# Performance work log

Hardware: AMD Instinct MI355X
Metric: run time of the kernel (lower is better)

## Reference

```python
import jax, jax.numpy as jnp
import numpy as np

N = 100000   # nodes
E = 1600000  # directed edges
D = 128      # feature dim (input = hidden = embedding)
LN_EPS = 1e-5


def setup_inputs() -> dict:
    key = jax.random.key(0)
    ks = jax.random.split(key, 8)
    scale = 1.0 / np.sqrt(D)
    x = jax.random.normal(ks[0], (N, D), dtype=jnp.float32)
    edge_index = jax.random.randint(ks[1], (2, E), 0, N, dtype=jnp.int64)
    W0 = jax.random.normal(ks[2], (D, D), dtype=jnp.float32) * scale
    W1 = jax.random.normal(ks[3], (D, D), dtype=jnp.float32) * scale
    W2 = jax.random.normal(ks[4], (D, D), dtype=jnp.float32) * scale
    b0 = jnp.zeros((D,), jnp.float32)
    b1 = jnp.zeros((D,), jnp.float32)
    b2 = jnp.zeros((D,), jnp.float32)
    ln_g = jnp.ones((D,), jnp.float32)
    ln_b = jnp.zeros((D,), jnp.float32)
    fn_g = jnp.ones((D,), jnp.float32)
    fn_b = jnp.zeros((D,), jnp.float32)
    return {"x": x, "edge_index": edge_index, "W0": W0, "b0": b0,
            "W1": W1, "b1": b1, "W2": W2, "b2": b2,
            "ln_g": ln_g, "ln_b": ln_b, "fn_g": fn_g, "fn_b": fn_b}


def _gcn_conv(x, W, b, src, dst, n):
    # PyG GCNConv: x' = D^{-1/2} (A + I) D^{-1/2} (x W) + b
    h = x @ W                                   # [N, D]
    # add self-loops
    loops = jnp.arange(n, dtype=src.dtype)
    s = jnp.concatenate([src, loops])           # source nodes
    d = jnp.concatenate([dst, loops])           # target nodes
    deg = jax.ops.segment_sum(jnp.ones_like(d, dtype=h.dtype), d, num_segments=n)
    dinv = jnp.where(deg > 0, jax.lax.rsqrt(deg), 0.0)
    norm = dinv[s] * dinv[d]                    # [E+N]
    msg = h[s] * norm[:, None]                  # gather + scale
    out = jax.ops.segment_sum(msg, d, num_segments=n)  # scatter-add at targets
    return out + b


def _layer_norm(x, g, b):
    mu = jnp.mean(x, axis=-1, keepdims=True)
    var = jnp.mean(jnp.square(x - mu), axis=-1, keepdims=True)
    return (x - mu) * jax.lax.rsqrt(var + LN_EPS) * g + b


def reference(x, edge_index, W0, b0, W1, b1, W2, b2, ln_g, ln_b, fn_g, fn_b):
    src, dst = edge_index[0], edge_index[1]
    n = x.shape[0]
    h = jax.nn.relu(_gcn_conv(x, W0, b0, src, dst, n))
    # single middle block (num_gnn_layers=3 -> loop runs for i=1 only)
    identity = h
    h = _layer_norm(h, ln_g, ln_b)
    h = jax.nn.relu(_gcn_conv(h, W1, b1, src, dst, n)) + identity
    h = _gcn_conv(h, W2, b2, src, dst, n)
    return _layer_norm(h, fn_g, fn_b)
```

## Files before the change

### kernel.cpp

```cpp
#include <hip/hip_runtime.h>
#include <hip/hip_bf16.h>

#define DIM 128
#define SB 256
#define NA 256
#define EAMAX 6272
#define BCAP 4096

typedef __attribute__((ext_vector_type(8))) short bf16x8;
typedef __attribute__((ext_vector_type(4))) float f32x4;

__device__ inline float bf2f(unsigned short u) {
    unsigned v = (unsigned)u << 16;
    union { unsigned u; float f; } c; c.u = v; return c.f;
}
__device__ inline unsigned short f2bf(float f) {
    union { __hip_bfloat16 h; unsigned short u; } c;
    c.h = __float2bfloat16(f);
    return c.u;
}
__device__ inline unsigned pk2(float a, float b) {
    return (unsigned)f2bf(a) | ((unsigned)f2bf(b) << 16);
}


__global__ __launch_bounds__(256) void k_hist(const int* __restrict__ dst,
                                              int* __restrict__ histG,
                                              int E, int EA, int nbuk) {
    __shared__ int h[1024];
    int t = threadIdx.x, blk = blockIdx.x;
    for (int i = t; i < 1024; i += 256) h[i] = 0;
    __syncthreads();
    int lo = blk * EA, hi = min(E, lo + EA);
    for (int i = lo + t; i < hi; i += 256) atomicAdd(&h[dst[i] >> 7], 1);
    __syncthreads();
    for (int bk = t; bk < nbuk; bk += 256) histG[bk * NA + blk] = h[bk];
}

__global__ __launch_bounds__(SB) void k_scan1(const int* __restrict__ cnt,
                                              int* __restrict__ bsum, int n) {
    int t = threadIdx.x;
    int i = blockIdx.x * SB + t;
    int v = (i < n) ? cnt[i] : 0;
#pragma unroll
    for (int m = 1; m < 64; m <<= 1) v += __shfl_xor(v, m);
    __shared__ int w[SB / 64];
    if ((t & 63) == 0) w[t >> 6] = v;
    __syncthreads();
    if (t == 0) {
        int s = 0;
#pragma unroll
        for (int k = 0; k < SB / 64; ++k) s += w[k];
        bsum[blockIdx.x] = s;
    }
}

__global__ __launch_bounds__(1024) void k_scan2(int* __restrict__ bsum, int B) {
    __shared__ int s[1024];
    int t = threadIdx.x;
    int v = (t < B) ? bsum[t] : 0;
    s[t] = v;
    __syncthreads();
    for (int off = 1; off < 1024; off <<= 1) {
        int u = (t >= off) ? s[t - off] : 0;
        __syncthreads();
        s[t] += u;
        __syncthreads();
    }
    if (t < B) bsum[t] = s[t] - v;
}

__global__ __launch_bounds__(SB) void k_scan3g(const int* __restrict__ cnt,
                                               const int* __restrict__ bsum,
                                               int* __restrict__ outx, int n) {
    __shared__ int s[SB];
    int t = threadIdx.x;
    int i = blockIdx.x * SB + t;
    int c = (i < n) ? cnt[i] : 0;
    s[t] = c;
    __syncthreads();
    for (int off = 1; off < SB; off <<= 1) {
        int u = (t >= off) ? s[t - off] : 0;
        __syncthreads();
        s[t] += u;
        __syncthreads();
    }
    int excl = bsum[blockIdx.x] + s[t] - c;
    if (i < n) {
        outx[i] = excl;
        if (i == n - 1) outx[n] = excl + c;
    }
}

__global__ __launch_bounds__(256) void k_place(const int* __restrict__ src,
                                               const int* __restrict__ dst,
                                               const int* __restrict__ scannedG,
                                               unsigned* __restrict__ ebuf,
                                               int E, int EA, int nbuk) {
    __shared__ int h[1024];
    __shared__ int dl[1024];
    __shared__ int ws4[4];
    __shared__ unsigned srt[EAMAX];
    __shared__ unsigned short bkt[EAMAX];
    int t = threadIdx.x, blk = blockIdx.x;
    int lo = blk * EA, hi = min(E, lo + EA);

    for (int i = t; i < 1024; i += 256) h[i] = 0;
    __syncthreads();
    for (int i = lo + t; i < hi; i += 256) atomicAdd(&h[dst[i] >> 7], 1);
    __syncthreads();

    {
        int b4 = t * 4;
        int v0 = h[b4], v1 = h[b4 + 1], v2 = h[b4 + 2], v3 = h[b4 + 3];
        int i1 = v0 + v1, i2 = i1 + v2, i3 = i2 + v3;
        int lane = t & 63, wv = t >> 6;
        int sc = i3;
#pragma unroll
        for (int o = 1; o < 64; o <<= 1) {
            int u = __shfl_up(sc, o);
            if (lane >= o) sc += u;
        }
        if (lane == 63) ws4[wv] = sc;
        __syncthreads();
        int woff = 0;
#pragma unroll
        for (int k = 0; k < 4; ++k) woff += (k < wv) ? ws4[k] : 0;
        int tex = woff + sc - i3;
        h[b4] = tex; h[b4 + 1] = tex + v0; h[b4 + 2] = tex + i1; h[b4 + 3] = tex + i2;
    }
    __syncthreads();

    for (int bk = t; bk < nbuk; bk += 256)
        dl[bk] = scannedG[bk * NA + blk] - h[bk];
    __syncthreads();

    for (int i = lo + t; i < hi; i += 256) {
        int d = dst[i];
        int bk = d >> 7;
        unsigned p = ((unsigned)(d & 127) << 17) | (unsigned)src[i];
        int r = atomicAdd(&h[bk], 1);
        srt[r] = p;
        bkt[r] = (unsigned short)bk;
    }
    __syncthreads();

    int m = hi - lo;
    for (int i = t; i < m; i += 256)
        ebuf[dl[bkt[i]] + i] = srt[i];
}

__global__ __launch_bounds__(256) void k_finish(const unsigned* __restrict__ ebuf,
                                                const int* __restrict__ scannedG,
                                                int* __restrict__ offs,
                                                float* __restrict__ dinv,
                                                int* __restrict__ csrc,
                                                int n, int nbuk) {
    __shared__ unsigned eds[BCAP];
    __shared__ unsigned srt[BCAP];
    __shared__ int lcnt[128], lcur[128];
    __shared__ int wsum[2];
    int b = blockIdx.x, t = threadIdx.x;
    int e0 = scannedG[b * NA], e1 = scannedG[(b + 1) * NA];
    int m = min(e1 - e0, BCAP);

    for (int i = t; i < m; i += 256) eds[i] = ebuf[e0 + i];
    if (t < 128) lcnt[t] = 0;
    __syncthreads();
    for (int i = t; i < m; i += 256) atomicAdd(&lcnt[eds[i] >> 17], 1);
    __syncthreads();

    int c = (t < 128) ? lcnt[t] : 0;
    int lane = t & 63, wv = t >> 6;
    int s = c;
#pragma unroll
    for (int o = 1; o < 64; o <<= 1) {
        int u = __shfl_up(s, o);
        if (lane >= o) s += u;
    }
    if (lane == 63 && wv < 2) wsum[wv] = s;
    __syncthreads();
    int excl = s - c + ((wv == 1) ? wsum[0] : 0);
    if (t < 128) {
        int node = b * 128 + t;
        if (node < n) {
            offs[node] = e0 + excl;
            dinv[node] = rsqrtf((float)(c + 1));
        }
        lcur[t] = excl;
    }
    if (b == nbuk - 1 && t == 0) offs[n] = e1;
    __syncthreads();

    for (int i = t; i < m; i += 256) {
        unsigned v = eds[i];
        int r = atomicAdd(&lcur[v >> 17], 1);
        srt[r] = v & 0x1FFFFu;
    }
    __syncthreads();
    for (int i = t; i < m; i += 256) csrc[e0 + i] = (int)srt[i];
}


template <int BF>
__global__ __launch_bounds__(256) void k_gemm(const void* __restrict__ inp,
                                              const float* __restrict__ W,
                                              const float* __restrict__ dinv,
                                              unsigned short* __restrict__ outH, int n) {
    __shared__ unsigned short Wt[DIM * 136];
    int t = threadIdx.x;
#pragma unroll
    for (int i = 0; i < 64; ++i) {
        int idx = i * 256 + t;
        int k = idx >> 7, nn = idx & 127;
        Wt[nn * 136 + k] = f2bf(W[idx]);
    }
    __syncthreads();

    int l = t & 63, w = t >> 6;
    int g = l >> 4, li = l & 15;
    int rbase = blockIdx.x * 128 + w * 32;

    f32x4 acc[2][8];
#pragma unroll
    for (int mt = 0; mt < 2; ++mt)
#pragma unroll
        for (int nt = 0; nt < 8; ++nt) acc[mt][nt] = (f32x4)(0.f);

#pragma unroll
    for (int kk = 0; kk < 4; ++kk) {
        bf16x8 a[2];
#pragma unroll
        for (int mt = 0; mt < 2; ++mt) {
            int row = rbase + mt * 16 + li;
            int rr = (row < n) ? row : (n - 1);
            if (BF) {
                const unsigned short* pb =
                    (const unsigned short*)inp + (size_t)rr * DIM + kk * 32 + g * 8;
                a[mt] = *(const bf16x8*)pb;
            } else {
                const float* p = (const float*)inp + (size_t)rr * DIM + kk * 32 + g * 8;
                float4 v0 = *(const float4*)p;
                float4 v1 = *(const float4*)(p + 4);
                bf16x8 av;
                av[0] = (short)f2bf(v0.x); av[1] = (short)f2bf(v0.y);
                av[2] = (short)f2bf(v0.z); av[3] = (short)f2bf(v0.w);
                av[4] = (short)f2bf(v1.x); av[5] = (short)f2bf(v1.y);
                av[6] = (short)f2bf(v1.z); av[7] = (short)f2bf(v1.w);
                a[mt] = av;
            }
        }
#pragma unroll
        for (int nt = 0; nt < 8; ++nt) {
            bf16x8 bb = *(const bf16x8*)&Wt[(nt * 16 + li) * 136 + kk * 32 + g * 8];
            acc[0][nt] = __builtin_amdgcn_mfma_f32_16x16x32_bf16(a[0], bb, acc[0][nt], 0, 0, 0);
            acc[1][nt] = __builtin_amdgcn_mfma_f32_16x16x32_bf16(a[1], bb, acc[1][nt], 0, 0, 0);
        }
    }

#pragma unroll
    for (int mt = 0; mt < 2; ++mt)
#pragma unroll
        for (int r = 0; r < 4; ++r) {
            int row = rbase + mt * 16 + g * 4 + r;
            if (row < n) {
                float s = dinv[row];
#pragma unroll
                for (int nt = 0; nt < 8; ++nt)
                    outH[(size_t)row * DIM + nt * 16 + li] = f2bf(acc[mt][nt][r] * s);
            }
        }
}


template <int MODE>
__global__ __launch_bounds__(256) void k_agg(const unsigned* __restrict__ H2,
                                             const float* __restrict__ dinv,
                                             const int* __restrict__ offs,
                                             const int* __restrict__ csrc,
                                             const float* __restrict__ bias,
                                             const unsigned* __restrict__ idbf,
                                             unsigned* __restrict__ rawbf,
                                             unsigned* __restrict__ lnbf,
                                             float* __restrict__ outf,
                                             const float* __restrict__ lg,
                                             const float* __restrict__ lb, int n) {
    int wv = threadIdx.x >> 6, lane = threadIdx.x & 63;
    int i = blockIdx.x * 4 + wv;
    if (i >= n) return;

    unsigned u0 = H2[(size_t)i * 64 + lane];
    float ax = bf2f((unsigned short)(u0 & 0xffff));
    float ay = bf2f((unsigned short)(u0 >> 16));

    int s = offs[i], e = offs[i + 1];
    int j = s;
    for (; j + 16 <= e; j += 16) {
        int idx[16];
#pragma unroll
        for (int q = 0; q < 16; ++q) idx[q] = csrc[j + q];
        unsigned uu[16];
#pragma unroll
        for (int q = 0; q < 16; ++q) uu[q] = H2[(size_t)idx[q] * 64 + lane];
#pragma unroll
        for (int q = 0; q < 16; ++q) {
            ax += bf2f((unsigned short)(uu[q] & 0xffff));
            ay += bf2f((unsigned short)(uu[q] >> 16));
        }
    }
    for (; j + 4 <= e; j += 4) {
        unsigned uu[4];
#pragma unroll
        for (int q = 0; q < 4; ++q) uu[q] = H2[(size_t)csrc[j + q] * 64 + lane];
#pragma unroll
        for (int q = 0; q < 4; ++q) {
            ax += bf2f((unsigned short)(uu[q] & 0xffff));
            ay += bf2f((unsigned short)(uu[q] >> 16));
        }
    }
    for (; j < e; ++j) {
        unsigned v = H2[(size_t)csrc[j] * 64 + lane];
        ax += bf2f((unsigned short)(v & 0xffff));
        ay += bf2f((unsigned short)(v >> 16));
    }

    float di = dinv[i];
    float2 bs = ((const float2*)bias)[lane];
    float vx = di * ax + bs.x;
    float vy = di * ay + bs.y;

    float xx, xy;
    if (MODE == 0) { xx = fmaxf(vx, 0.f); xy = fmaxf(vy, 0.f); }
    if (MODE == 1) {
        unsigned idu = idbf[(size_t)i * 64 + lane];
        xx = fmaxf(vx, 0.f) + bf2f((unsigned short)(idu & 0xffff));
        xy = fmaxf(vy, 0.f) + bf2f((unsigned short)(idu >> 16));
    }
    if (MODE == 2) { xx = vx; xy = vy; }

    if (MODE == 0 || MODE == 1)
        rawbf[(size_t)i * 64 + lane] = pk2(xx, xy);

    if (MODE == 0 || MODE == 2) {
        float su = xx + xy;
#pragma unroll
        for (int m = 1; m < 64; m <<= 1) su += __shfl_xor(su, m);
        float mu = su * (1.f / 128.f);
        float dx = xx - mu, dy = xy - mu;
        float q = dx * dx + dy * dy;
#pragma unroll
        for (int m = 1; m < 64; m <<= 1) q += __shfl_xor(q, m);
        float rstd = rsqrtf(q * (1.f / 128.f) + 1e-5f);
        float2 gg = ((const float2*)lg)[lane];
        float2 bb2 = ((const float2*)lb)[lane];
        float ox = dx * rstd * gg.x + bb2.x;
        float oy = dy * rstd * gg.y + bb2.y;
        if (MODE == 0)
            lnbf[(size_t)i * 64 + lane] = pk2(ox, oy);
        else
            ((float2*)(outf + (size_t)i * DIM))[lane] = make_float2(ox, oy);
    }
}


static inline char* alignp(char* p) {
    return (char*)(((size_t)p + 255) & ~(size_t)255);
}

extern "C" void kernel_launch(void* const* d_in, const int* in_sizes, int n_in,
                              void* d_out, int out_size, void* d_ws, size_t ws_size,
                              hipStream_t stream) {
    const float* x   = (const float*)d_in[0];
    const int*   ei  = (const int*)d_in[1];
    const float* W0  = (const float*)d_in[2];
    const float* b0  = (const float*)d_in[3];
    const float* W1  = (const float*)d_in[4];
    const float* b1  = (const float*)d_in[5];
    const float* W2  = (const float*)d_in[6];
    const float* b2  = (const float*)d_in[7];
    const float* lng = (const float*)d_in[8];
    const float* lnb = (const float*)d_in[9];
    const float* fng = (const float*)d_in[10];
    const float* fnb = (const float*)d_in[11];
    float* out = (float*)d_out;

    int n = in_sizes[0] / DIM;
    int E = in_sizes[1] / 2;
    const int* src = ei;
    const int* dst = ei + E;

    int nbuk = (n + 127) >> 7;
    int EA   = (E + NA - 1) / NA;
    int nh   = nbuk * NA;

    char* p = (char*)d_ws;
    unsigned short* H  = (unsigned short*)p; p = alignp(p + (size_t)n * DIM * 2);
    unsigned* hb  = (unsigned*)p;            p = alignp(p + (size_t)n * DIM * 2);
    unsigned* lno = (unsigned*)p;            p = alignp(p + (size_t)n * DIM * 2);
    float* dinv = (float*)p;                 p = alignp(p + (size_t)n * 4);
    int*   offs = (int*)p;                   p = alignp(p + (size_t)(n + 1) * 4);
    int*   csrc = (int*)p;                   p = alignp(p + (size_t)E * 4);
    unsigned* ebuf = (unsigned*)p;           p = alignp(p + (size_t)E * 4);
    int*   histG = (int*)p;                  p = alignp(p + (size_t)nh * 4);
    int*   scannedG = (int*)p;               p = alignp(p + (size_t)(nh + 1) * 4);
    int*   bsum = (int*)p;

    int grid_g = (n + 127) / 128;
    int Bs = (nh + SB - 1) / SB;

    k_hist<<<NA, 256, 0, stream>>>(dst, histG, E, EA, nbuk);
    k_scan1<<<Bs, SB, 0, stream>>>(histG, bsum, nh);
    k_scan2<<<1, 1024, 0, stream>>>(bsum, Bs);
    k_scan3g<<<Bs, SB, 0, stream>>>(histG, bsum, scannedG, nh);
    k_place<<<NA, 256, 0, stream>>>(src, dst, scannedG, ebuf, E, EA, nbuk);
    k_finish<<<nbuk, 256, 0, stream>>>(ebuf, scannedG, offs, dinv, csrc, n, nbuk);

    const unsigned* H2 = (const unsigned*)H;
    int grid_a = (n + 3) / 4;

    k_gemm<0><<<grid_g, 256, 0, stream>>>(x, W0, dinv, H, n);
    k_agg<0><<<grid_a, 256, 0, stream>>>(H2, dinv, offs, csrc, b0, nullptr,
                                         hb, lno, nullptr, lng, lnb, n);

    k_gemm<1><<<grid_g, 256, 0, stream>>>(lno, W1, dinv, H, n);
    k_agg<1><<<grid_a, 256, 0, stream>>>(H2, dinv, offs, csrc, b1, hb,
                                         hb, nullptr, nullptr, nullptr, nullptr, n);

    k_gemm<1><<<grid_g, 256, 0, stream>>>(hb, W2, dinv, H, n);
    k_agg<2><<<grid_a, 256, 0, stream>>>(H2, dinv, offs, csrc, b2, nullptr,
                                         nullptr, nullptr, out, fng, fnb, n);
}
```

Measured before the change: 332.0 us.

## Split gather wave into two half-waves with 8-byte loads; fuse scan1 into histogram

```diff
diff --git a/kernel.cpp b/kernel.cpp
--- a/kernel.cpp
+++ b/kernel.cpp
@@ -26,6 +26,7 @@
 
 __global__ __launch_bounds__(256) void k_hist(const int* __restrict__ dst,
                                               int* __restrict__ histG,
+                                              int* __restrict__ bsum,
                                               int E, int EA, int nbuk) {
     __shared__ int h[1024];
     int t = threadIdx.x, blk = blockIdx.x;
@@ -34,24 +35,10 @@
     int lo = blk * EA, hi = min(E, lo + EA);
     for (int i = lo + t; i < hi; i += 256) atomicAdd(&h[dst[i] >> 7], 1);
     __syncthreads();
-    for (int bk = t; bk < nbuk; bk += 256) histG[bk * NA + blk] = h[bk];
-}
-
-__global__ __launch_bounds__(SB) void k_scan1(const int* __restrict__ cnt,
-                                              int* __restrict__ bsum, int n) {
-    int t = threadIdx.x;
-    int i = blockIdx.x * SB + t;
-    int v = (i < n) ? cnt[i] : 0;
-#pragma unroll
-    for (int m = 1; m < 64; m <<= 1) v += __shfl_xor(v, m);
-    __shared__ int w[SB / 64];
-    if ((t & 63) == 0) w[t >> 6] = v;
-    __syncthreads();
-    if (t == 0) {
-        int s = 0;
-#pragma unroll
-        for (int k = 0; k < SB / 64; ++k) s += w[k];
-        bsum[blockIdx.x] = s;
+    for (int bk = t; bk < nbuk; bk += 256) {
+        int c = h[bk];
+        histG[bk * NA + blk] = c;
+        if (c) atomicAdd(&bsum[bk], c);
     }
 }
 
@@ -288,77 +275,105 @@
     int wv = threadIdx.x >> 6, lane = threadIdx.x & 63;
     int i = blockIdx.x * 4 + wv;
     if (i >= n) return;
-
-    unsigned u0 = H2[(size_t)i * 64 + lane];
-    float ax = bf2f((unsigned short)(u0 & 0xffff));
-    float ay = bf2f((unsigned short)(u0 >> 16));
+    int g = lane >> 5;
+    int c = lane & 31;
+
+    const uint2* Hp = (const uint2*)H2;
+
+    float a0 = 0.f, a1 = 0.f, a2 = 0.f, a3 = 0.f;
+    if (g == 0) {
+        uint2 u = Hp[(size_t)i * 32 + c];
+        a0 = bf2f((unsigned short)(u.x & 0xffff));
+        a1 = bf2f((unsigned short)(u.x >> 16));
+        a2 = bf2f((unsigned short)(u.y & 0xffff));
+        a3 = bf2f((unsigned short)(u.y >> 16));
+    }
 
     int s = offs[i], e = offs[i + 1];
     int j = s;
     for (; j + 16 <= e; j += 16) {
-        int idx[16];
-#pragma unroll
-        for (int q = 0; q < 16; ++q) idx[q] = csrc[j + q];
-        unsigned uu[16];
-#pragma unroll
-        for (int q = 0; q < 16; ++q) uu[q] = H2[(size_t)idx[q] * 64 + lane];
-#pragma unroll
-        for (int q = 0; q < 16; ++q) {
-            ax += bf2f((unsigned short)(uu[q] & 0xffff));
-            ay += bf2f((unsigned short)(uu[q] >> 16));
-        }
-    }
-    for (; j + 4 <= e; j += 4) {
-        unsigned uu[4];
-#pragma unroll
-        for (int q = 0; q < 4; ++q) uu[q] = H2[(size_t)csrc[j + q] * 64 + lane];
-#pragma unroll
-        for (int q = 0; q < 4; ++q) {
-            ax += bf2f((unsigned short)(uu[q] & 0xffff));
-            ay += bf2f((unsigned short)(uu[q] >> 16));
-        }
-    }
-    for (; j < e; ++j) {
-        unsigned v = H2[(size_t)csrc[j] * 64 + lane];
-        ax += bf2f((unsigned short)(v & 0xffff));
-        ay += bf2f((unsigned short)(v >> 16));
-    }
+        int idx[8];
+#pragma unroll
+        for (int q = 0; q < 8; ++q) idx[q] = csrc[j + 2 * q + g];
+        uint2 uu[8];
+#pragma unroll
+        for (int q = 0; q < 8; ++q) uu[q] = Hp[(size_t)idx[q] * 32 + c];
+#pragma unroll
+        for (int q = 0; q < 8; ++q) {
+            a0 += bf2f((unsigned short)(uu[q].x & 0xffff));
+            a1 += bf2f((unsigned short)(uu[q].x >> 16));
+            a2 += bf2f((unsigned short)(uu[q].y & 0xffff));
+            a3 += bf2f((unsigned short)(uu[q].y >> 16));
+        }
+    }
+    for (; j + 2 <= e; j += 2) {
+        uint2 u = Hp[(size_t)csrc[j + g] * 32 + c];
+        a0 += bf2f((unsigned short)(u.x & 0xffff));
+        a1 += bf2f((unsigned short)(u.x >> 16));
+        a2 += bf2f((unsigned short)(u.y & 0xffff));
+        a3 += bf2f((unsigned short)(u.y >> 16));
+    }
+    if (j < e && g == 0) {
+        uint2 u = Hp[(size_t)csrc[j] * 32 + c];
+        a0 += bf2f((unsigned short)(u.x & 0xffff));
+        a1 += bf2f((unsigned short)(u.x >> 16));
+        a2 += bf2f((unsigned short)(u.y & 0xffff));
+        a3 += bf2f((unsigned short)(u.y >> 16));
+    }
+
+    a0 += __shfl_xor(a0, 32);
+    a1 += __shfl_xor(a1, 32);
+    a2 += __shfl_xor(a2, 32);
+    a3 += __shfl_xor(a3, 32);
 
     float di = dinv[i];
-    float2 bs = ((const float2*)bias)[lane];
-    float vx = di * ax + bs.x;
-    float vy = di * ay + bs.y;
-
-    float xx, xy;
-    if (MODE == 0) { xx = fmaxf(vx, 0.f); xy = fmaxf(vy, 0.f); }
+    float4 bs = ((const float4*)bias)[c];
+    float v0 = di * a0 + bs.x;
+    float v1 = di * a1 + bs.y;
+    float v2 = di * a2 + bs.z;
+    float v3 = di * a3 + bs.w;
+
+    float x0, x1, x2, x3;
+    if (MODE == 0) {
+        x0 = fmaxf(v0, 0.f); x1 = fmaxf(v1, 0.f);
+        x2 = fmaxf(v2, 0.f); x3 = fmaxf(v3, 0.f);
+    }
     if (MODE == 1) {
-        unsigned idu = idbf[(size_t)i * 64 + lane];
-        xx = fmaxf(vx, 0.f) + bf2f((unsigned short)(idu & 0xffff));
-        xy = fmaxf(vy, 0.f) + bf2f((unsigned short)(idu >> 16));
-    }
-    if (MODE == 2) { xx = vx; xy = vy; }
-
-    if (MODE == 0 || MODE == 1)
-        rawbf[(size_t)i * 64 + lane] = pk2(xx, xy);
+        uint2 idu = ((const uint2*)idbf)[(size_t)i * 32 + c];
+        x0 = fmaxf(v0, 0.f) + bf2f((unsigned short)(idu.x & 0xffff));
+        x1 = fmaxf(v1, 0.f) + bf2f((unsigned short)(idu.x >> 16));
+        x2 = fmaxf(v2, 0.f) + bf2f((unsigned short)(idu.y & 0xffff));
+        x3 = fmaxf(v3, 0.f) + bf2f((unsigned short)(idu.y >> 16));
+    }
+    if (MODE == 2) { x0 = v0; x1 = v1; x2 = v2; x3 = v3; }
+
+    if (MODE == 0 || MODE == 1) {
+        if (g == 0)
+            ((uint2*)rawbf)[(size_t)i * 32 + c] = make_uint2(pk2(x0, x1), pk2(x2, x3));
+    }
 
     if (MODE == 0 || MODE == 2) {
-        float su = xx + xy;
-#pragma unroll
-        for (int m = 1; m < 64; m <<= 1) su += __shfl_xor(su, m);
+        float su = x0 + x1 + x2 + x3;
+#pragma unroll
+        for (int m = 1; m < 32; m <<= 1) su += __shfl_xor(su, m);
         float mu = su * (1.f / 128.f);
-        float dx = xx - mu, dy = xy - mu;
-        float q = dx * dx + dy * dy;
-#pragma unroll
-        for (int m = 1; m < 64; m <<= 1) q += __shfl_xor(q, m);
+        float d0 = x0 - mu, d1 = x1 - mu, d2 = x2 - mu, d3 = x3 - mu;
+        float q = d0 * d0 + d1 * d1 + d2 * d2 + d3 * d3;
+#pragma unroll
+        for (int m = 1; m < 32; m <<= 1) q += __shfl_xor(q, m);
         float rstd = rsqrtf(q * (1.f / 128.f) + 1e-5f);
-        float2 gg = ((const float2*)lg)[lane];
-        float2 bb2 = ((const float2*)lb)[lane];
-        float ox = dx * rstd * gg.x + bb2.x;
-        float oy = dy * rstd * gg.y + bb2.y;
-        if (MODE == 0)
-            lnbf[(size_t)i * 64 + lane] = pk2(ox, oy);
-        else
-            ((float2*)(outf + (size_t)i * DIM))[lane] = make_float2(ox, oy);
+        float4 gg = ((const float4*)lg)[c];
+        float4 bb = ((const float4*)lb)[c];
+        float o0 = d0 * rstd * gg.x + bb.x;
+        float o1 = d1 * rstd * gg.y + bb.y;
+        float o2 = d2 * rstd * gg.z + bb.z;
+        float o3 = d3 * rstd * gg.w + bb.w;
+        if (g == 0) {
+            if (MODE == 0)
+                ((uint2*)lnbf)[(size_t)i * 32 + c] = make_uint2(pk2(o0, o1), pk2(o2, o3));
+            else
+                ((float4*)outf)[(size_t)i * 32 + c] = make_float4(o0, o1, o2, o3);
+        }
     }
 }
 
@@ -408,9 +423,9 @@
     int grid_g = (n + 127) / 128;
     int Bs = (nh + SB - 1) / SB;
 
-    k_hist<<<NA, 256, 0, stream>>>(dst, histG, E, EA, nbuk);
-    k_scan1<<<Bs, SB, 0, stream>>>(histG, bsum, nh);
-    k_scan2<<<1, 1024, 0, stream>>>(bsum, Bs);
+    hipMemsetAsync(bsum, 0, (size_t)nbuk * sizeof(int), stream);
+    k_hist<<<NA, 256, 0, stream>>>(dst, histG, bsum, E, EA, nbuk);
+    k_scan2<<<1, 1024, 0, stream>>>(bsum, nbuk);
     k_scan3g<<<Bs, SB, 0, stream>>>(histG, bsum, scannedG, nh);
     k_place<<<NA, 256, 0, stream>>>(src, dst, scannedG, ebuf, E, EA, nbuk);
     k_finish<<<nbuk, 256, 0, stream>>>(ebuf, scannedG, offs, dinv, csrc, n, nbuk);
```

New measurement: 382.6 us. +15.2%, slower.
